# Kernel tuning notes

Hardware: AMD Instinct MI355X
Metric: run time of the kernel (lower is better)

The kernel has to match this reference:

```python
import jax, jax.numpy as jnp
import numpy as np

B, WIN, H, A, K, NAPP = 32768, 100, 64, 64, 8, 4
DT = 0.1
LN_EPS = 1e-5


def _layernorm(x, w, b):
    m = jnp.mean(x, axis=-1, keepdims=True)
    v = jnp.mean(jnp.square(x - m), axis=-1, keepdims=True)
    return (x - m) * jax.lax.rsqrt(v + LN_EPS) * w + b


def setup_inputs() -> dict:
    key = jax.random.key(0)
    ks = jax.random.split(key, 12)
    xav = float(np.sqrt(6.0 / (H + H)))  # xavier_uniform for lnn_rec
    return {
        "y": jax.random.normal(ks[0], (B, WIN), dtype=jnp.float32),
        "w_in": jax.random.normal(ks[1], (H,), dtype=jnp.float32) * 0.5,  # Linear(1,H) weight
        "b_in": jax.random.normal(ks[2], (H,), dtype=jnp.float32) * 0.1,
        "tau_param": jnp.ones((H,), dtype=jnp.float32),
        "W_rec": jax.random.uniform(ks[3], (H, H), dtype=jnp.float32, minval=-xav, maxval=xav),
        "ln_w": jnp.ones((H,), dtype=jnp.float32),
        "ln_b": jnp.zeros((H,), dtype=jnp.float32),
        "Wx0": jax.random.normal(ks[4], (A, H), dtype=jnp.float32) * 0.1,
        "bx0": jnp.zeros((A,), dtype=jnp.float32),
        "We": jax.random.normal(ks[5], (K, A, WIN), dtype=jnp.float32) * 0.1,
        "be": jnp.zeros((K, A), dtype=jnp.float32),
        "Wr": jax.random.normal(ks[6], (K, A, A), dtype=jnp.float32) * 0.1,
        "thr": jnp.full((K, A), 0.1, dtype=jnp.float32),
        "head_W": jax.random.normal(ks[7], (NAPP, A), dtype=jnp.float32) * 0.1,
        "head_b": jnp.zeros((NAPP,), dtype=jnp.float32),
    }


def reference(y, w_in, b_in, tau_param, W_rec, ln_w, ln_b, Wx0, bx0, We, be, Wr, thr, head_W, head_b):
    batch = y.shape[0]
    tau = jax.nn.softplus(tau_param)  # (H,)

    def step(h, x_t):
        # x_t: (B,) scalar input per sample; Linear(1,H): x_t * w_in + b_in
        pre = x_t[:, None] * w_in + b_in + h @ W_rec  # (B,H)
        f_t = jnp.tanh(_layernorm(pre, ln_w, ln_b))
        dh = (-h / tau + f_t) * DT
        h_new = jnp.clip(h + dh, -10.0, 10.0)
        return h_new, None

    h0 = jnp.zeros((batch, H), dtype=y.dtype)
    h, _ = jax.lax.scan(step, h0, y.T)

    x = h @ Wx0.T + bx0  # (B,A) warm start
    for k in range(K):
        z = y @ We[k].T + be[k] + x @ Wr[k].T  # (B,A)
        lam = jax.nn.softplus(thr[k])
        x = jnp.sign(z) * jnp.maximum(jnp.abs(z) - lam, 0.0)

    power = x @ head_W.T + head_b  # (B,NAPP) — cat of per-appliance 1-out heads
    return power, x
```

## Files before the change

kernel.cpp:

```cpp
#include <hip/hip_runtime.h>


#define NB 32768
#define WIN 100
#define HH 64
#define AA 64
#define KITER 8
#define NAPPC 4
#define LNEPS 1e-5f
#define DTC 0.1f

#define WS_WREC 0
#define WS_WE   8192
#define WS_WR   139264
#define WS_WC   204800
#define WS_BC   205056
#define WS_DEC  205312
#define WS_LAM  205568

typedef _Float16 f16x8 __attribute__((ext_vector_type(8)));
typedef _Float16 f16x4 __attribute__((ext_vector_type(4)));
typedef _Float16 f16x2v __attribute__((ext_vector_type(2)));
typedef __fp16 fp16x2 __attribute__((ext_vector_type(2)));
typedef float f32x4 __attribute__((ext_vector_type(4)));

union H4 { f16x4 v; fp16x2 h[2]; };
union HS8 { f16x2v p[4]; f16x8 v; };
union FD { f16x2v h; fp16x2 u; };

__device__ __forceinline__ float exp2_fast(float x) { return __builtin_amdgcn_exp2f(x); }
__device__ __forceinline__ float rsq_fast(float x) { return __builtin_amdgcn_rsqf(x); }
__device__ __forceinline__ float log2_fast(float x) { return __builtin_amdgcn_logf(x); }
__device__ __forceinline__ float softplus_fast(float x) {
  float ax = fabsf(x);
  float e = exp2_fast(-ax * 1.4426950408889634f);
  return fmaxf(x, 0.0f) + log2_fast(1.0f + e) * 0.6931471805599453f;
}
__device__ __forceinline__ f16x2v pk2(float a, float b) {
  FD t;
  t.u = __builtin_amdgcn_cvt_pkrtz(a, b);
  return t.h;
}
__device__ __forceinline__ f16x4 pack4(float a, float b, float c2, float d) {
  H4 t;
  t.h[0] = __builtin_amdgcn_cvt_pkrtz(a, b);
  t.h[1] = __builtin_amdgcn_cvt_pkrtz(c2, d);
  return t.v;
}
__device__ __forceinline__ f16x8 pack8(float a, float b, float c2, float d,
                                       float e, float f, float g2, float h) {
  HS8 t;
  t.p[0] = pk2(a, b);
  t.p[1] = pk2(c2, d);
  t.p[2] = pk2(e, f);
  t.p[3] = pk2(g2, h);
  return t.v;
}
__device__ __forceinline__ float fdot2f(f16x2v a, f16x2v b, float c) {
  FD A, B;
  A.h = a;
  B.h = b;
  return __builtin_amdgcn_fdot2(A.u, B.u, c, false);
}
__device__ __forceinline__ f16x2v rcp2(f16x2v d) {
  f16x2v r;
  r[0] = __builtin_amdgcn_rcph(d[0]);
  r[1] = __builtin_amdgcn_rcph(d[1]);
  return r;
}
__device__ __forceinline__ float xreduce(float q) {
  q += __shfl_xor(q, 16);
  q += __shfl_xor(q, 32);
  return q;
}

__global__ __launch_bounds__(256) void pinn_prep(
    const float* __restrict__ W_rec, const float* __restrict__ w_in,
    const float* __restrict__ b_in, const float* __restrict__ tau,
    const float* __restrict__ thr, const float* __restrict__ We,
    const float* __restrict__ Wr, char* __restrict__ ws) {
  _Float16* wrec16 = (_Float16*)(ws + WS_WREC);
  _Float16* we16 = (_Float16*)(ws + WS_WE);
  _Float16* wr16 = (_Float16*)(ws + WS_WR);
  float* wc = (float*)(ws + WS_WC);
  float* bc = (float*)(ws + WS_BC);
  float* dec = (float*)(ws + WS_DEC);
  float* lam = (float*)(ws + WS_LAM);
  const int tid = threadIdx.x, bid = blockIdx.x;
  if (bid == 0) {
    __shared__ float rm[64];
    if (tid < 64) {
      float s = 0.f;
      for (int m = 0; m < 64; ++m) s += W_rec[tid * 64 + m];
      rm[tid] = s * (1.f / 64.f);
    }
    __syncthreads();
    for (int idx = tid; idx < 4096; idx += 256) {
      const int j = idx & 7, l = (idx >> 3) & 63, kt = (idx >> 9) & 1, mt = idx >> 10;
      const int g4 = ((l >> 4) << 2);
      const int k_in = kt * 32 + ((j < 4) ? (g4 + j) : (16 + g4 + (j - 4)));
      const int m = mt * 16 + (l & 15);
      wrec16[idx] = (_Float16)(W_rec[k_in * 64 + m] - rm[k_in]);
    }
    if (tid < 64) {
      float sw = 0.f, sb = 0.f;
      for (int i = 0; i < 64; ++i) { sw += w_in[i]; sb += b_in[i]; }
      wc[tid] = w_in[tid] - sw * (1.f / 64.f);
      bc[tid] = b_in[tid] - sb * (1.f / 64.f);
      dec[tid] = 1.f - DTC / softplus_fast(tau[tid]);
    }
    for (int i = tid; i < 512; i += 256) lam[i] = softplus_fast(thr[i]);
  } else {
    const int stride = (gridDim.x - 1) * 256;
    for (int i = (bid - 1) * 256 + tid; i < 65536 + 32768; i += stride) {
      if (i < 65536) {
        const int j = i & 7, l = (i >> 3) & 63, kt = (i >> 9) & 3, mt = (i >> 11) & 3, k = i >> 13;
        const int g4 = ((l >> 4) << 2);
        const int t = kt * 32 + ((j < 4) ? (g4 + j) : (16 + g4 + (j - 4)));
        const int row = k * 64 + mt * 16 + (l & 15);
        we16[i] = (t < WIN) ? (_Float16)We[row * WIN + t] : (_Float16)0.f;
      } else {
        const int i2 = i - 65536;
        const int j = i2 & 7, l = (i2 >> 3) & 63, kt = (i2 >> 9) & 1, mt = (i2 >> 10) & 3, k = i2 >> 12;
        const int g4 = ((l >> 4) << 2);
        const int k_in = kt * 32 + ((j < 4) ? (g4 + j) : (16 + g4 + (j - 4)));
        const int row = k * 64 + mt * 16 + (l & 15);
        wr16[i2] = (_Float16)Wr[row * 64 + k_in];
      }
    }
  }
}

__global__ __attribute__((amdgpu_flat_work_group_size(64, 64),
                          amdgpu_waves_per_eu(2, 2))) void pinn_fused(
    const float* __restrict__ y, const float* __restrict__ ln_w,
    const float* __restrict__ ln_b, const float* __restrict__ Wx0,
    const float* __restrict__ bx0, const float* __restrict__ be,
    const float* __restrict__ head_W, const float* __restrict__ head_b,
    const char* __restrict__ ws, float* __restrict__ out) {
  __shared__ float ybuf[16][101];

  const _Float16* wrec16 = (const _Float16*)(ws + WS_WREC);
  const _Float16* we16 = (const _Float16*)(ws + WS_WE);
  const _Float16* wr16 = (const _Float16*)(ws + WS_WR);
  const float* wcp = (const float*)(ws + WS_WC);
  const float* bcp = (const float*)(ws + WS_BC);
  const float* decp = (const float*)(ws + WS_DEC);
  const float* lamp = (const float*)(ws + WS_LAM);

  const int l = threadIdx.x;
  const int c = l & 15;
  const int g = l >> 4;
  const int s0 = blockIdx.x * 16;

  for (int i = l; i < 16 * WIN; i += 64) {
    const int s = i / WIN;
    ybuf[s][i - s * WIN] = y[s0 * WIN + i];
  }

  f16x2v wc2[8], bc2[8], lnw2[8], lnb2[8], dec2[8];
#pragma unroll
  for (int mt = 0; mt < 4; ++mt) {
    const int hb4 = mt * 16 + g * 4;
    const float4 wi = *(const float4*)&wcp[hb4];
    const float4 bi = *(const float4*)&bcp[hb4];
    const float4 lw = *(const float4*)&ln_w[hb4];
    const float4 lb = *(const float4*)&ln_b[hb4];
    const float4 dc = *(const float4*)&decp[hb4];
    wc2[mt * 2] = pk2(wi.x, wi.y);
    wc2[mt * 2 + 1] = pk2(wi.z, wi.w);
    bc2[mt * 2] = pk2(bi.x, bi.y);
    bc2[mt * 2 + 1] = pk2(bi.z, bi.w);
    lnw2[mt * 2] = pk2(lw.x, lw.y);
    lnw2[mt * 2 + 1] = pk2(lw.z, lw.w);
    lnb2[mt * 2] = pk2(lb.x, lb.y);
    lnb2[mt * 2 + 1] = pk2(lb.z, lb.w);
    dec2[mt * 2] = pk2(dc.x, dc.y);
    dec2[mt * 2 + 1] = pk2(dc.z, dc.w);
  }

  f16x8 wrec32[4][2];
#pragma unroll
  for (int mt = 0; mt < 4; ++mt)
#pragma unroll
    for (int kt = 0; kt < 2; ++kt)
      wrec32[mt][kt] = *(const f16x8*)&wrec16[((mt * 2 + kt) * 64 + l) * 8];

  __syncthreads();

  f16x2v hs2[8];
#pragma unroll
  for (int i = 0; i < 8; ++i) hs2[i] = pk2(0.f, 0.f);
  f16x8 hbA, hbB;
  {
    HS8 u0, u1;
    u0.p[0] = hs2[0]; u0.p[1] = hs2[1]; u0.p[2] = hs2[2]; u0.p[3] = hs2[3];
    u1.p[0] = hs2[4]; u1.p[1] = hs2[5]; u1.p[2] = hs2[6]; u1.p[3] = hs2[7];
    hbA = u0.v;
    hbB = u1.v;
  }
  const float inv64 = 1.0f / 64.0f;

  const f16x2v c0p1n = pk2(0.1f, 0.1f);
  const f16x2v c1p5 = pk2(1.5f, 1.5f);
  const f16x2v c6 = pk2(6.f, 6.f);
  const f16x2v c15 = pk2(15.f, 15.f);
  const f16x2v cP = pk2(0.1f, 0.1f);
  const f16x2v cM = pk2(-0.1f, -0.1f);
  const f16x2v c10 = pk2(10.f, 10.f);
  const f16x2v cm10 = pk2(-10.f, -10.f);
  const f16x4 ones4 = pack4(1.f, 1.f, 1.f, 1.f);

  float xt = ybuf[c][0];
  for (int t = 0; t < WIN; ++t) {
    const float xtn = ybuf[c][t + 1];
    const f16x2v xtv = pk2(xt, xt);
    f32x4 acc[4];
#pragma unroll
    for (int mt = 0; mt < 4; ++mt) {
      f32x4 a = {0.f, 0.f, 0.f, 0.f};
      a = __builtin_amdgcn_mfma_f32_16x16x32_f16(wrec32[mt][0], hbA, a, 0, 0, 0);
      a = __builtin_amdgcn_mfma_f32_16x16x32_f16(wrec32[mt][1], hbB, a, 0, 0, 0);
      acc[mt] = a;
    }
    f16x2v pre2[8];
    float q0 = 0.f, q1 = 0.f;
#pragma unroll
    for (int mt = 0; mt < 4; ++mt)
#pragma unroll
      for (int p = 0; p < 2; ++p) {
        const int i = mt * 2 + p;
        const f16x2v d = pk2(acc[mt][2 * p], acc[mt][2 * p + 1]);
        const f16x2v tb = __builtin_elementwise_fma(xtv, wc2[i], bc2[i]);
        const f16x2v pre = d + tb;
        pre2[i] = pre;
        if (i < 4) q0 = fdot2f(pre, pre, q0);
        else q1 = fdot2f(pre, pre, q1);
      }
    const float q4 = (q0 + q1) * 0.25f;
    const f16x4 qB = pack4(q4, q4, q4, q4);
    f32x4 sv = {0.f, 0.f, 0.f, 0.f};
    sv = __builtin_amdgcn_mfma_f32_16x16x16f16(ones4, qB, sv, 0, 0, 0);
    const float rstd = rsq_fast(fmaf(sv[0], inv64, LNEPS));
    const f16x2v rstdv = pk2(rstd, rstd);
#pragma unroll
    for (int i = 0; i < 8; ++i) {
      const f16x2v u = __builtin_elementwise_fma(pre2[i] * rstdv, lnw2[i], lnb2[i]);
      const f16x2v x2 = u * u;
      const f16x2v n1 = __builtin_elementwise_fma(x2, c0p1n, c1p5);
      const f16x2v num = u * n1;
      const f16x2v den = __builtin_elementwise_fma(x2, c6, c15);
      f16x2v tt = num * rcp2(den);
      tt = __builtin_elementwise_min(tt, cP);
      tt = __builtin_elementwise_max(tt, cM);
      f16x2v h = __builtin_elementwise_fma(hs2[i], dec2[i], tt);
      h = __builtin_elementwise_min(h, c10);
      h = __builtin_elementwise_max(h, cm10);
      hs2[i] = h;
    }
    {
      HS8 u0, u1;
      u0.p[0] = hs2[0]; u0.p[1] = hs2[1]; u0.p[2] = hs2[2]; u0.p[3] = hs2[3];
      u1.p[0] = hs2[4]; u1.p[1] = hs2[5]; u1.p[2] = hs2[6]; u1.p[3] = hs2[7];
      hbA = u0.v;
      hbB = u1.v;
    }
    xt = xtn;
  }

  float xs[16];
#pragma unroll
  for (int mt = 0; mt < 4; ++mt) {
    const float4 b4 = *(const float4*)&bx0[mt * 16 + 4 * g];
    f32x4 a = {b4.x, b4.y, b4.z, b4.w};
#pragma unroll
    for (int kt = 0; kt < 2; ++kt) {
      const float4 w0 = *(const float4*)&Wx0[(mt * 16 + c) * HH + kt * 32 + 4 * g];
      const float4 w1 = *(const float4*)&Wx0[(mt * 16 + c) * HH + kt * 32 + 16 + 4 * g];
      const f16x8 wf = pack8(w0.x, w0.y, w0.z, w0.w, w1.x, w1.y, w1.z, w1.w);
      a = __builtin_amdgcn_mfma_f32_16x16x32_f16(wf, (kt == 0) ? hbA : hbB, a, 0, 0, 0);
    }
#pragma unroll
    for (int r = 0; r < 4; ++r) xs[mt * 4 + r] = a[r];
  }
  f16x8 xb8[2];
  xb8[0] = pack8(xs[0], xs[1], xs[2], xs[3], xs[4], xs[5], xs[6], xs[7]);
  xb8[1] = pack8(xs[8], xs[9], xs[10], xs[11], xs[12], xs[13], xs[14], xs[15]);

  f16x8 yf8[4];
#pragma unroll
  for (int kt = 0; kt < 4; ++kt) {
    float v[8];
#pragma unroll
    for (int j = 0; j < 8; ++j) {
      const int t = kt * 32 + ((j < 4) ? (4 * g + j) : (16 + 4 * g + (j - 4)));
      v[j] = (t < WIN) ? ybuf[c][t] : 0.f;
    }
    yf8[kt] = pack8(v[0], v[1], v[2], v[3], v[4], v[5], v[6], v[7]);
  }

  for (int k = 0; k < KITER; ++k) {
    f32x4 z[4];
#pragma unroll
    for (int mt = 0; mt < 4; ++mt) {
      const float4 be4 = *(const float4*)&be[k * AA + mt * 16 + 4 * g];
      f32x4 a = {be4.x, be4.y, be4.z, be4.w};
      const int baseWe = (((k * 4 + mt) * 4) * 64 + l) * 8;
#pragma unroll
      for (int kt = 0; kt < 4; ++kt) {
        const f16x8 wf = *(const f16x8*)&we16[baseWe + kt * 512];
        a = __builtin_amdgcn_mfma_f32_16x16x32_f16(wf, yf8[kt], a, 0, 0, 0);
      }
      const int baseWr = (((k * 4 + mt) * 2) * 64 + l) * 8;
#pragma unroll
      for (int kt = 0; kt < 2; ++kt) {
        const f16x8 wf = *(const f16x8*)&wr16[baseWr + kt * 512];
        a = __builtin_amdgcn_mfma_f32_16x16x32_f16(wf, xb8[kt], a, 0, 0, 0);
      }
      z[mt] = a;
    }
#pragma unroll
    for (int mt = 0; mt < 4; ++mt) {
      const float4 lm4 = *(const float4*)&lamp[k * AA + mt * 16 + 4 * g];
      float xv[4];
#pragma unroll
      for (int r = 0; r < 4; ++r) {
        const float zz = z[mt][r];
        const float v = fmaxf(fabsf(zz) - (&lm4.x)[r], 0.0f);
        xv[r] = copysignf(v, zz);
        xs[mt * 4 + r] = xv[r];
      }
    }
    xb8[0] = pack8(xs[0], xs[1], xs[2], xs[3], xs[4], xs[5], xs[6], xs[7]);
    xb8[1] = pack8(xs[8], xs[9], xs[10], xs[11], xs[12], xs[13], xs[14], xs[15]);
  }

  float* __restrict__ outp = out;
  float* __restrict__ outx = out + NB * NAPPC;
#pragma unroll
  for (int mt = 0; mt < 4; ++mt) {
    float4 v;
#pragma unroll
    for (int r = 0; r < 4; ++r) (&v.x)[r] = xs[mt * 4 + r];
    *(float4*)&outx[(s0 + c) * AA + mt * 16 + 4 * g] = v;
  }

  float P[4];
#pragma unroll
  for (int p = 0; p < NAPPC; ++p) {
    float acc = 0.f;
#pragma unroll
    for (int mt = 0; mt < 4; ++mt) {
      const float4 hw = *(const float4*)&head_W[p * AA + mt * 16 + 4 * g];
#pragma unroll
      for (int r = 0; r < 4; ++r) acc = fmaf(xs[mt * 4 + r], (&hw.x)[r], acc);
    }
    acc = xreduce(acc);
    P[p] = acc + head_b[p];
  }
  if (g == 0) {
    float4 pv;
#pragma unroll
    for (int p = 0; p < 4; ++p) (&pv.x)[p] = P[p];
    *(float4*)&outp[(s0 + c) * NAPPC] = pv;
  }
}

extern "C" void kernel_launch(void* const* d_in, const int* in_sizes, int n_in,
                              void* d_out, int out_size, void* d_ws, size_t ws_size,
                              hipStream_t stream) {
  const float* y         = (const float*)d_in[0];
  const float* w_in      = (const float*)d_in[1];
  const float* b_in      = (const float*)d_in[2];
  const float* tau_param = (const float*)d_in[3];
  const float* W_rec     = (const float*)d_in[4];
  const float* ln_w      = (const float*)d_in[5];
  const float* ln_b      = (const float*)d_in[6];
  const float* Wx0       = (const float*)d_in[7];
  const float* bx0       = (const float*)d_in[8];
  const float* We        = (const float*)d_in[9];
  const float* be        = (const float*)d_in[10];
  const float* Wr        = (const float*)d_in[11];
  const float* thr       = (const float*)d_in[12];
  const float* head_W    = (const float*)d_in[13];
  const float* head_b    = (const float*)d_in[14];

  pinn_prep<<<dim3(90), dim3(256), 0, stream>>>(
      W_rec, w_in, b_in, tau_param, thr, We, Wr, (char*)d_ws);
  pinn_fused<<<dim3(NB / 16), dim3(64), 0, stream>>>(
      y, ln_w, ln_b, Wx0, bx0, be, head_W, head_b, (const char*)d_ws,
      (float*)d_out);
}
```

Measured before the change: 110.7 us.

## Fold input projection into MFMA accumulator and drop clamp in recurrence

Seeds the MFMA accumulator with the fp32 input projection (x_t*w_in+b_in), which removes the separate packed-half FMA and add per element. The sum-of-squares reduction now uses four independent dot chains and a 16x16x32 MFMA broadcast instead of 16x16x16. It also removes the ±10 clamp on h, relying on the bounded update (|tt|≤0.1 with decay) to keep h in range, and unrolls the time loop by 2. Dropping the clamp assumes it can never be active, which changes semantics only if h could otherwise exceed 10.

```diff
diff --git a/kernel.cpp b/kernel.cpp
--- a/kernel.cpp
+++ b/kernel.cpp
@@ -158,7 +158,8 @@
     ybuf[s][i - s * WIN] = y[s0 * WIN + i];
   }
 
-  f16x2v wc2[8], bc2[8], lnw2[8], lnb2[8], dec2[8];
+  float wcf[16], bcf[16];
+  f16x2v lnw2[8], lnb2[8], dec2[8];
 #pragma unroll
   for (int mt = 0; mt < 4; ++mt) {
     const int hb4 = mt * 16 + g * 4;
@@ -167,10 +168,11 @@
     const float4 lw = *(const float4*)&ln_w[hb4];
     const float4 lb = *(const float4*)&ln_b[hb4];
     const float4 dc = *(const float4*)&decp[hb4];
-    wc2[mt * 2] = pk2(wi.x, wi.y);
-    wc2[mt * 2 + 1] = pk2(wi.z, wi.w);
-    bc2[mt * 2] = pk2(bi.x, bi.y);
-    bc2[mt * 2 + 1] = pk2(bi.z, bi.w);
+#pragma unroll
+    for (int r = 0; r < 4; ++r) {
+      wcf[mt * 4 + r] = (&wi.x)[r];
+      bcf[mt * 4 + r] = (&bi.x)[r];
+    }
     lnw2[mt * 2] = pk2(lw.x, lw.y);
     lnw2[mt * 2 + 1] = pk2(lw.z, lw.w);
     lnb2[mt * 2] = pk2(lb.x, lb.y);
@@ -207,40 +209,48 @@
   const f16x2v c15 = pk2(15.f, 15.f);
   const f16x2v cP = pk2(0.1f, 0.1f);
   const f16x2v cM = pk2(-0.1f, -0.1f);
-  const f16x2v c10 = pk2(10.f, 10.f);
-  const f16x2v cm10 = pk2(-10.f, -10.f);
-  const f16x4 ones4 = pack4(1.f, 1.f, 1.f, 1.f);
+  const f16x8 ones8 = pack8(1.f, 1.f, 1.f, 1.f, 1.f, 1.f, 1.f, 1.f);
 
   float xt = ybuf[c][0];
+#pragma unroll 2
   for (int t = 0; t < WIN; ++t) {
     const float xtn = ybuf[c][t + 1];
-    const f16x2v xtv = pk2(xt, xt);
     f32x4 acc[4];
 #pragma unroll
     for (int mt = 0; mt < 4; ++mt) {
-      f32x4 a = {0.f, 0.f, 0.f, 0.f};
+      f32x4 a;
+#pragma unroll
+      for (int r = 0; r < 4; ++r) a[r] = fmaf(xt, wcf[mt * 4 + r], bcf[mt * 4 + r]);
       a = __builtin_amdgcn_mfma_f32_16x16x32_f16(wrec32[mt][0], hbA, a, 0, 0, 0);
       a = __builtin_amdgcn_mfma_f32_16x16x32_f16(wrec32[mt][1], hbB, a, 0, 0, 0);
       acc[mt] = a;
     }
     f16x2v pre2[8];
-    float q0 = 0.f, q1 = 0.f;
-#pragma unroll
-    for (int mt = 0; mt < 4; ++mt)
-#pragma unroll
-      for (int p = 0; p < 2; ++p) {
-        const int i = mt * 2 + p;
-        const f16x2v d = pk2(acc[mt][2 * p], acc[mt][2 * p + 1]);
-        const f16x2v tb = __builtin_elementwise_fma(xtv, wc2[i], bc2[i]);
-        const f16x2v pre = d + tb;
-        pre2[i] = pre;
-        if (i < 4) q0 = fdot2f(pre, pre, q0);
-        else q1 = fdot2f(pre, pre, q1);
-      }
-    const float q4 = (q0 + q1) * 0.25f;
-    const f16x4 qB = pack4(q4, q4, q4, q4);
+#pragma unroll
+    for (int mt = 0; mt < 4; ++mt) {
+      pre2[mt * 2] = pk2(acc[mt][0], acc[mt][1]);
+      pre2[mt * 2 + 1] = pk2(acc[mt][2], acc[mt][3]);
+    }
+    float qa = fdot2f(pre2[0], pre2[0], 0.f);
+    float qb = fdot2f(pre2[2], pre2[2], 0.f);
+    float qc = fdot2f(pre2[4], pre2[4], 0.f);
+    float qd = fdot2f(pre2[6], pre2[6], 0.f);
+    qa = fdot2f(pre2[1], pre2[1], qa);
+    qb = fdot2f(pre2[3], pre2[3], qb);
+    qc = fdot2f(pre2[5], pre2[5], qc);
+    qd = fdot2f(pre2[7], pre2[7], qd);
+    const float q8 = ((qa + qb) + (qc + qd)) * 0.125f;
+    f16x8 qB;
+    {
+      HS8 u;
+      u.p[0] = pk2(q8, q8);
+      u.p[1] = u.p[0];
+      u.p[2] = u.p[0];
+      u.p[3] = u.p[0];
+      qB = u.v;
+    }
     f32x4 sv = {0.f, 0.f, 0.f, 0.f};
-    sv = __builtin_amdgcn_mfma_f32_16x16x16f16(ones4, qB, sv, 0, 0, 0);
+    sv = __builtin_amdgcn_mfma_f32_16x16x32_f16(ones8, qB, sv, 0, 0, 0);
     const float rstd = rsq_fast(fmaf(sv[0], inv64, LNEPS));
     const f16x2v rstdv = pk2(rstd, rstd);
 #pragma unroll
@@ -253,10 +263,7 @@
       f16x2v tt = num * rcp2(den);
       tt = __builtin_elementwise_min(tt, cP);
       tt = __builtin_elementwise_max(tt, cM);
-      f16x2v h = __builtin_elementwise_fma(hs2[i], dec2[i], tt);
-      h = __builtin_elementwise_min(h, c10);
-      h = __builtin_elementwise_max(h, cm10);
-      hs2[i] = h;
+      hs2[i] = __builtin_elementwise_fma(hs2[i], dec2[i], tt);
     }
     {
       HS8 u0, u1;
```

Result: faster. 100.5 us (-9.2%).
